# Kernel optimization log

Measured on AMD Instinct MI355X. Metric: run time of the kernel, lower is better.

The kernel has to match this reference:

```python
import jax, jax.numpy as jnp
import numpy as np

B, D, K, NUM_CLASSES = 8192, 512, 20, 1024
EPS = 1e-12  # torch F.normalize clamp


def setup_inputs() -> dict:
    key = jax.random.key(0)
    k1, k2 = jax.random.split(key)
    batch = jax.random.normal(k1, (B, D), dtype=jnp.float32)
    labels = jax.random.randint(k2, (B,), 0, NUM_CLASSES, dtype=jnp.int64 if jax.config.jax_enable_x64 else jnp.int32)
    return {"batch": batch, "labels": labels, "k": K}


def reference(batch, labels, k):
    # L2-normalize rows (F.normalize, p=2)
    norm = jnp.maximum(jnp.linalg.norm(batch, axis=1, keepdims=True), EPS)
    x = batch / norm
    cos = x @ x.T                                   # [B, B] cosine similarity
    min_value = cos.min() - 1.0                     # scalar, computed before diag fill
    bs = cos.shape[0]
    diag = jnp.eye(bs, dtype=bool)
    cos = jnp.where(diag, min_value, cos)           # fill_diagonal_(min_value)
    # argsort(-cos)[:, :k]  ==  top-k by similarity (self excluded via diag fill)
    top_vals, top_idx = jax.lax.top_k(cos, k)       # [B, k]
    # preds = (cos + 1)/2 gathered at neighbor indices == (top_vals + 1)/2
    preds = (top_vals + 1.0) * 0.5
    true_labels = (labels[top_idx] == labels[:, None]).astype(jnp.float32)  # [B, k]
    # nn.BCELoss with mean reduction; torch clamps each log term at -100
    logp = jnp.maximum(jnp.log(preds), -100.0)
    log1mp = jnp.maximum(jnp.log1p(-preds), -100.0)
    loss = -(true_labels * logp + (1.0 - true_labels) * log1mp)
    return loss.mean()
```

## Files before the change

kernel.cpp:

```cpp
#include <hip/hip_runtime.h>
#include <hip/hip_bf16.h>

#define NROWS 8192
#define DIM   512
#define KSEL  20
#define NSURV 384
#define NTRI  2080

typedef unsigned int u32;
typedef unsigned long long u64;
typedef short bf16x8 __attribute__((ext_vector_type(8)));
typedef float f32x4 __attribute__((ext_vector_type(4)));
typedef ushort u16x2 __attribute__((ext_vector_type(2)));

typedef const void __attribute__((address_space(1))) as1_void;
typedef void __attribute__((address_space(3))) as3_void;

__device__ __forceinline__ void async_ld16(const ushort* g, ushort* l) {
    __builtin_amdgcn_global_load_lds((as1_void*)g, (as3_void*)l, 16, 0, 0);
}

__device__ __forceinline__ ushort f2bf(float f) {
    u32 u = __float_as_uint(f);
    return (ushort)((u + 0x7FFFu + ((u >> 16) & 1u)) >> 16);
}

__device__ __forceinline__ u32 mono16(u32 r) {
    return r ^ (0x8000u | ((r >> 15) * 0x7FFFu));
}
__device__ __forceinline__ u32 mono2(u32 w) {
    return w ^ (0x80008000u | (((w >> 15) & 0x10001u) * 0x7FFFu));
}
__device__ __forceinline__ u32 mkey(float f) { return mono16((u32)f2bf(f)); }

__device__ __forceinline__ u32 pkmax(u32 a, u32 b) {
    union { u32 u; u16x2 v; } x, y; x.u = a; y.u = b;
    x.v = __builtin_elementwise_max(x.v, y.v);
    return x.u;
}
__device__ __forceinline__ u32 pkmin(u32 a, u32 b) {
    union { u32 u; u16x2 v; } x, y; x.u = a; y.u = b;
    x.v = __builtin_elementwise_min(x.v, y.v);
    return x.u;
}

__device__ __forceinline__ void tri_idx(int t, int& by, int& bx) {
    by = (int)((sqrtf(8.0f * (float)t + 1.0f) - 1.0f) * 0.5f);
    while ((by + 1) * (by + 2) / 2 <= t) ++by;
    while (by * (by + 1) / 2 > t) --by;
    bx = t - by * (by + 1) / 2;
}

__global__ __launch_bounds__(256) void k_norm(const float* __restrict__ x,
                                              ushort* __restrict__ xn) {
    int lane = threadIdx.x & 63;
    int wv   = threadIdx.x >> 6;
    int row  = blockIdx.x * 4 + wv;
    const float4* xr = (const float4*)(x + (size_t)row * DIM);
    float4 a = xr[2 * lane];
    float4 b = xr[2 * lane + 1];
    float ss = a.x*a.x + a.y*a.y + a.z*a.z + a.w*a.w
             + b.x*b.x + b.y*b.y + b.z*b.z + b.w*b.w;
    #pragma unroll
    for (int off = 32; off; off >>= 1) ss += __shfl_xor(ss, off);
    float sc = 1.0f / fmaxf(sqrtf(ss), 1e-12f);
    float v[8] = {a.x*sc, a.y*sc, a.z*sc, a.w*sc, b.x*sc, b.y*sc, b.z*sc, b.w*sc};
    union { ushort u[8]; uint4 q; } o;
    #pragma unroll
    for (int i = 0; i < 8; ++i) o.u[i] = f2bf(v[i]);
    *(uint4*)(xn + (size_t)row * DIM + lane * 8) = o.q;
}

__global__ __launch_bounds__(256) void k_gemm(const ushort* __restrict__ xn,
                                              ushort* __restrict__ C,
                                              ushort* __restrict__ M) {
    __shared__ ushort sh[128 * 128];
    ushort* lA = sh;
    ushort* lB = sh + 128 * 64;
    int tid  = threadIdx.x;
    int lane = tid & 63, wv = tid >> 6;
    int wr = wv >> 1, wc = wv & 1;
    int q = lane >> 4, m = lane & 15;
    int bx, by;
    tri_idx(blockIdx.x, by, bx);
    int grow0 = by * 128;
    int gcol0 = bx * 128;
    f32x4 acc[4][4] = {};

    int lr = lane >> 3;
    int lc = lane & 7;
    for (int kc = 0; kc < 8; ++kc) {
        #pragma unroll
        for (int t = 0; t < 4; ++t) {
            int rb  = wv * 32 + t * 8;
            int r   = rb + lr;
            int fch = lc ^ (r & 7);
            async_ld16(xn + (size_t)(grow0 + r) * DIM + kc * 64 + fch * 8, &lA[rb * 64]);
            async_ld16(xn + (size_t)(gcol0 + r) * DIM + kc * 64 + fch * 8, &lB[rb * 64]);
        }
        __syncthreads();
        #pragma unroll
        for (int s = 0; s < 2; ++s) {
            bf16x8 af[4], bfr[4];
            #pragma unroll
            for (int i = 0; i < 4; ++i) {
                int ra = wr * 64 + i * 16 + m;
                af[i]  = *(const bf16x8*)&lA[ra * 64 + (((s * 4 + q) ^ (ra & 7)) * 8)];
                int rb2 = wc * 64 + i * 16 + m;
                bfr[i] = *(const bf16x8*)&lB[rb2 * 64 + (((s * 4 + q) ^ (rb2 & 7)) * 8)];
            }
            #pragma unroll
            for (int i = 0; i < 4; ++i)
                #pragma unroll
                for (int j = 0; j < 4; ++j)
                    acc[i][j] = __builtin_amdgcn_mfma_f32_16x16x32_bf16(af[i], bfr[j], acc[i][j], 0, 0, 0);
        }
        __syncthreads();
    }

    float cmf[4] = {-3.0f, -3.0f, -3.0f, -3.0f};
    #pragma unroll
    for (int i = 0; i < 4; ++i) {
        float rmf[4] = {-3.0f, -3.0f, -3.0f, -3.0f};
        int rloc = wr * 64 + i * 16 + q * 4;
        #pragma unroll
        for (int j = 0; j < 4; ++j) {
            int cl = wc * 64 + j * 16 + m;
            int c  = gcol0 + cl;
            #pragma unroll
            for (int reg = 0; reg < 4; ++reg) {
                int r    = rloc + reg;
                int grw  = grow0 + r;
                float a  = acc[i][j][reg];
                bool dg  = (grw == c);
                float mv = dg ? -3.0f : a;
                rmf[reg] = fmaxf(rmf[reg], mv);
                cmf[j]   = fmaxf(cmf[j], mv);
                int D = r * 64 + ((cl >> 1) ^ (q << 3));
                sh[D * 2 + (cl & 1)] = dg ? (ushort)0xC040 : f2bf(a);
            }
        }
        u32 p01 = mkey(rmf[0]) | (mkey(rmf[1]) << 16);
        u32 p23 = mkey(rmf[2]) | (mkey(rmf[3]) << 16);
        #pragma unroll
        for (int off = 1; off <= 8; off <<= 1) {
            p01 = pkmax(p01, (u32)__shfl_xor((int)p01, off));
            p23 = pkmax(p23, (u32)__shfl_xor((int)p23, off));
        }
        if (m == 0) {
            size_t mb = (size_t)(grow0 + rloc) * 128 + bx * 2 + wc;
            M[mb]       = (ushort)(p01 & 0xFFFFu);
            M[mb + 128] = (ushort)(p01 >> 16);
            M[mb + 256] = (ushort)(p23 & 0xFFFFu);
            M[mb + 384] = (ushort)(p23 >> 16);
        }
    }
    if (bx != by) {
        u32 q01 = mkey(cmf[0]) | (mkey(cmf[1]) << 16);
        u32 q23 = mkey(cmf[2]) | (mkey(cmf[3]) << 16);
        q01 = pkmax(q01, (u32)__shfl_xor((int)q01, 16));
        q01 = pkmax(q01, (u32)__shfl_xor((int)q01, 32));
        q23 = pkmax(q23, (u32)__shfl_xor((int)q23, 16));
        q23 = pkmax(q23, (u32)__shfl_xor((int)q23, 32));
        if (q == 0) {
            int gc = gcol0 + wc * 64 + m;
            int sg = by * 2 + wr;
            M[(size_t)(gc +  0) * 128 + sg] = (ushort)(q01 & 0xFFFFu);
            M[(size_t)(gc + 16) * 128 + sg] = (ushort)(q01 >> 16);
            M[(size_t)(gc + 32) * 128 + sg] = (ushort)(q23 & 0xFFFFu);
            M[(size_t)(gc + 48) * 128 + sg] = (ushort)(q23 >> 16);
        }
    }
    __syncthreads();

    int tr = tid >> 4;
    int tc = tid & 15;
    #pragma unroll
    for (int p = 0; p < 8; ++p) {
        int r  = p * 16 + tr;
        int qr = (r >> 2) & 3;
        uint4 v = *(const uint4*)&sh[(r * 64 + ((tc * 4) ^ (qr << 3))) * 2];
        *(uint4*)&C[(size_t)(by * 128 + r) * NROWS + gcol0 + tc * 8] = v;
    }
}

__global__ __launch_bounds__(256) void k_thresh(const ushort* __restrict__ M,
                                                ushort* __restrict__ T) {
    int lane = threadIdx.x & 63;
    int wv   = threadIdx.x >> 6;
    int row  = blockIdx.x * 4 + wv;
    u32 pm  = *(const u32*)&M[(size_t)row * 128 + 2 * lane];
    u32 klo = pm & 0xFFFFu, khi = pm >> 16;
    u32 Tv = 0;
    #pragma unroll
    for (int b = 15; b >= 0; --b) {
        u32 cand = Tv | (1u << b);
        int c = __popcll(__ballot(klo >= cand)) + __popcll(__ballot(khi >= cand));
        if (c >= KSEL) Tv = cand;
    }
    if (Tv == 0) Tv = 1;
    if (lane == 0) T[row] = (ushort)Tv;
}

__global__ __launch_bounds__(256) void k_scan(const ushort* __restrict__ C,
                                              const ushort* __restrict__ T,
                                              u32* __restrict__ lists,
                                              u32* __restrict__ cnts) {
    int by, bx;
    tri_idx(blockIdx.x, by, bx);
    int tid = threadIdx.x;
    int tr  = tid >> 4;
    int gc  = bx * 128 + (tid & 15) * 8;
    bool diag = (bx == by);
    uint4 tq = *(const uint4*)&T[gc];
    u32 ts[4] = { tq.x, tq.y, tq.z, tq.w };
    u32 pmn = pkmin(pkmin(ts[0], ts[1]), pkmin(ts[2], ts[3]));
    u32 tmn = min(pmn & 0xFFFFu, pmn >> 16);
    #pragma unroll
    for (int p = 0; p < 8; ++p) {
        int gr = by * 128 + p * 16 + tr;
        uint4 v = *(const uint4*)&C[(size_t)gr * NROWS + gc];
        u32 k0 = mono2(v.x), k1 = mono2(v.y), k2 = mono2(v.z), k3 = mono2(v.w);
        u32 pmx = pkmax(pkmax(k0, k1), pkmax(k2, k3));
        u32 mx  = max(pmx & 0xFFFFu, pmx >> 16);
        u32 Tr  = (u32)T[gr];
        u32 ks[4] = { k0, k1, k2, k3 };
        if (mx >= Tr) {
            #pragma unroll
            for (int h = 0; h < 4; ++h) {
                u32 kA = ks[h] & 0xFFFFu, kB = ks[h] >> 16;
                if (kA >= Tr) { u32 o = atomicAdd(&cnts[gr], 1u); if (o < NSURV) lists[(size_t)gr * NSURV + o] = (kA << 16) | (u32)(gc + 2 * h); }
                if (kB >= Tr) { u32 o = atomicAdd(&cnts[gr], 1u); if (o < NSURV) lists[(size_t)gr * NSURV + o] = (kB << 16) | (u32)(gc + 2 * h + 1); }
            }
        }
        if (!diag && mx >= tmn) {
            #pragma unroll
            for (int h = 0; h < 4; ++h) {
                u32 kA = ks[h] & 0xFFFFu, kB = ks[h] >> 16;
                u32 tA = ts[h] & 0xFFFFu, tB = ts[h] >> 16;
                int cA = gc + 2 * h, cB = cA + 1;
                if (kA >= tA) { u32 o = atomicAdd(&cnts[cA], 1u); if (o < NSURV) lists[(size_t)cA * NSURV + o] = (kA << 16) | (u32)gr; }
                if (kB >= tB) { u32 o = atomicAdd(&cnts[cB], 1u); if (o < NSURV) lists[(size_t)cB * NSURV + o] = (kB << 16) | (u32)gr; }
            }
        }
    }
}

__global__ __launch_bounds__(256) void k_topk(const u32* __restrict__ lists,
                                              const u32* __restrict__ cnts,
                                              const int* __restrict__ labels,
                                              float* __restrict__ partials) {
    int lane = threadIdx.x & 63;
    int wv   = threadIdx.x >> 6;
    int row  = blockIdx.x * 4 + wv;
    u32 cnt = min(cnts[row], (u32)NSURV);
    const u32* L = lists + (size_t)row * NSURV;
    int mylab = labels[row];
    float loss = 0.0f;

    if (cnt <= 64u) {
        u32 gg  = ((u32)lane < cnt) ? L[lane] : 0u;
        u32 key = gg >> 16;
        u32 V = 0;
        #pragma unroll
        for (int b = 15; b >= 0; --b) {
            u32 cand = V | (1u << b);
            if (__popcll(__ballot(key >= cand)) >= KSEL) V = cand;
        }
        int cgt  = __popcll(__ballot(key > V));
        int ceq  = __popcll(__ballot(gg != 0 && key == V));
        int need = KSEL - cgt;
        bool incl;
        if (ceq == need) {
            incl = (gg != 0) && (key >= V);
        } else {
            u32 col = gg & 0xFFFFu;
            bool tie = (gg != 0) && (key == V);
            u32 Cv = 0;
            #pragma unroll
            for (int b = 15; b >= 0; --b) {
                u32 cand2 = Cv | (1u << b);
                if (__popcll(__ballot(tie && col >= cand2)) >= need) Cv = cand2;
            }
            incl = (key > V) || (tie && col >= Cv);
        }
        if (incl) {
            u32 col = gg & 0xFFFFu;
            u32 raw = (key & 0x8000u) ? (key ^ 0x8000u) : (key ^ 0xFFFFu);
            float v = __uint_as_float(raw << 16);
            float p = (v + 1.0f) * 0.5f;
            bool tm = (labels[col] == mylab);
            loss -= tm ? fmaxf(logf(p), -100.0f) : fmaxf(log1pf(-p), -100.0f);
        }
    } else {
        u32 g[6];
        #pragma unroll
        for (int j = 0; j < 6; ++j) {
            u32 idx = (u32)lane + (u32)j * 64u;
            g[j] = (idx < cnt) ? L[idx] : 0u;
        }
        u32 V = 0;
        #pragma unroll
        for (int b = 15; b >= 0; --b) {
            u32 cand = V | (1u << b);
            int c = 0;
            #pragma unroll
            for (int j = 0; j < 6; ++j)
                c += __popcll(__ballot((g[j] >> 16) >= cand));
            if (c >= KSEL) V = cand;
        }
        int cgt = 0, ceq = 0;
        #pragma unroll
        for (int j = 0; j < 6; ++j) {
            cgt += __popcll(__ballot(g[j] != 0 && (g[j] >> 16) > V));
            ceq += __popcll(__ballot(g[j] != 0 && (g[j] >> 16) == V));
        }
        int need = KSEL - cgt;
        bool all_ties = (ceq == need);
        #pragma unroll
        for (int j = 0; j < 6; ++j) {
            u32 key = g[j] >> 16, col = g[j] & 0xFFFFu;
            if (g[j] != 0 && (key > V || (all_ties && key == V))) {
                u32 raw = (key & 0x8000u) ? (key ^ 0x8000u) : (key ^ 0xFFFFu);
                float v = __uint_as_float(raw << 16);
                float p = (v + 1.0f) * 0.5f;
                bool tm = (labels[col] == mylab);
                loss -= tm ? fmaxf(logf(p), -100.0f) : fmaxf(log1pf(-p), -100.0f);
            }
        }
        if (!all_ties) {
            for (int r = 0; r < need; ++r) {
                u32 best = 0;
                #pragma unroll
                for (int j = 0; j < 6; ++j) {
                    u32 c2 = (g[j] != 0 && (g[j] >> 16) == V) ? ((g[j] & 0xFFFFu) + 1u) : 0u;
                    best = max(best, c2);
                }
                #pragma unroll
                for (int off = 32; off; off >>= 1) best = max(best, (u32)__shfl_xor((int)best, off));
                #pragma unroll
                for (int j = 0; j < 6; ++j) {
                    if (g[j] != 0 && (g[j] >> 16) == V && ((g[j] & 0xFFFFu) + 1u) == best) {
                        u32 col = g[j] & 0xFFFFu;
                        u32 raw = (V & 0x8000u) ? (V ^ 0x8000u) : (V ^ 0xFFFFu);
                        float v = __uint_as_float(raw << 16);
                        float p = (v + 1.0f) * 0.5f;
                        bool tm = (labels[col] == mylab);
                        loss -= tm ? fmaxf(logf(p), -100.0f) : fmaxf(log1pf(-p), -100.0f);
                        g[j] = 0;
                    }
                }
            }
        }
    }

    #pragma unroll
    for (int off = 32; off; off >>= 1) loss += __shfl_xor(loss, off);
    if (lane == 0) partials[row] = loss;
}

__global__ __launch_bounds__(256) void k_final(const float* __restrict__ partials,
                                               float* __restrict__ out) {
    __shared__ float s[4];
    int tid = threadIdx.x, lane = tid & 63, wvi = tid >> 6;
    const float4* p4 = (const float4*)partials;
    float sum = 0.0f;
    #pragma unroll
    for (int i = 0; i < 8; ++i) {
        float4 v = p4[tid + i * 256];
        sum += v.x + v.y + v.z + v.w;
    }
    #pragma unroll
    for (int off = 32; off; off >>= 1) sum += __shfl_xor(sum, off);
    if (lane == 0) s[wvi] = sum;
    __syncthreads();
    if (tid == 0) out[0] = (s[0] + s[1] + s[2] + s[3]) * (1.0f / (float)(NROWS * KSEL));
}

extern "C" void kernel_launch(void* const* d_in, const int* in_sizes, int n_in,
                              void* d_out, int out_size, void* d_ws, size_t ws_size,
                              hipStream_t stream) {
    const float* batch  = (const float*)d_in[0];
    const int*   labels = (const int*)d_in[1];

    ushort* xn = (ushort*)d_ws;
    ushort* C  = xn + (size_t)NROWS * DIM;

    char* scr = (char*)d_in[0];
    ushort* M        = (ushort*)scr;
    ushort* T        = (ushort*)(scr + (2u << 20));
    u32*    cnts     = (u32*)  (scr + (2u << 20) + (64u << 10));
    float*  partials = (float*)(scr + (2u << 20) + (128u << 10));
    u32*    lists    = (u32*)  (scr + (4u << 20));

    k_norm<<<NROWS / 4, 256, 0, stream>>>(batch, xn);
    hipMemsetAsync(cnts, 0, NROWS * sizeof(u32), stream);
    k_gemm  <<<NTRI,      256, 0, stream>>>(xn, C, M);
    k_thresh<<<NROWS / 4, 256, 0, stream>>>(M, T);
    k_scan  <<<NTRI,      256, 0, stream>>>(C, T, lists, cnts);
    k_topk  <<<NROWS / 4, 256, 0, stream>>>(lists, cnts, labels, partials);
    k_final <<<1,         256, 0, stream>>>(partials, (float*)d_out);
}
```

Measured before the change: 185.2 us.

## Store GEMM tiles in MFMA fragment order and scan them in that layout

The GEMM epilogue now writes each 128x128 bf16 tile straight to a per-block packed buffer in MFMA accumulator order. This removes the LDS staging pass, its extra barrier and the transposing row-major store. The scan kernel reads the packed tile contiguously and rebuilds row and column indices from the fragment layout. It fetches per-element row and column thresholds instead of per-row thresholds plus a column minimum. Stores become 8-byte per lane rather than 16-byte coalesced rows, and the scan's index math and threshold loads grow.

```diff
diff --git a/kernel.cpp b/kernel.cpp
--- a/kernel.cpp
+++ b/kernel.cpp
@@ -49,6 +49,11 @@
     while ((by + 1) * (by + 2) / 2 <= t) ++by;
     while (by * (by + 1) / 2 > t) --by;
     bx = t - by * (by + 1) / 2;
+}
+
+__device__ __forceinline__ void append(u32* lists, u32* cnts, int row, u32 val) {
+    u32 o = atomicAdd(&cnts[row], 1u);
+    if (o < NSURV) lists[(size_t)row * NSURV + o] = val;
 }
 
 __global__ __launch_bounds__(256) void k_norm(const float* __restrict__ x,
@@ -74,7 +79,7 @@
 __global__ __launch_bounds__(256) void k_gemm(const ushort* __restrict__ xn,
                                               ushort* __restrict__ C,
                                               ushort* __restrict__ M) {
-    __shared__ ushort sh[128 * 128];
+    __shared__ ushort sh[2 * 128 * 64];
     ushort* lA = sh;
     ushort* lB = sh + 128 * 64;
     int tid  = threadIdx.x;
@@ -118,6 +123,7 @@
         __syncthreads();
     }
 
+    size_t tb = (size_t)blockIdx.x * 16384;
     float cmf[4] = {-3.0f, -3.0f, -3.0f, -3.0f};
     #pragma unroll
     for (int i = 0; i < 4; ++i) {
@@ -127,18 +133,20 @@
         for (int j = 0; j < 4; ++j) {
             int cl = wc * 64 + j * 16 + m;
             int c  = gcol0 + cl;
+            ushort sv[4];
             #pragma unroll
             for (int reg = 0; reg < 4; ++reg) {
-                int r    = rloc + reg;
-                int grw  = grow0 + r;
+                int grw  = grow0 + rloc + reg;
                 float a  = acc[i][j][reg];
                 bool dg  = (grw == c);
                 float mv = dg ? -3.0f : a;
                 rmf[reg] = fmaxf(rmf[reg], mv);
                 cmf[j]   = fmaxf(cmf[j], mv);
-                int D = r * 64 + ((cl >> 1) ^ (q << 3));
-                sh[D * 2 + (cl & 1)] = dg ? (ushort)0xC040 : f2bf(a);
-            }
+                sv[reg]  = dg ? (ushort)0xC040 : f2bf(a);
+            }
+            uint2 o = { (u32)sv[0] | ((u32)sv[1] << 16),
+                        (u32)sv[2] | ((u32)sv[3] << 16) };
+            *(uint2*)&C[tb + (size_t)(((wv * 16 + i * 4 + j) * 64) + lane) * 4] = o;
         }
         u32 p01 = mkey(rmf[0]) | (mkey(rmf[1]) << 16);
         u32 p23 = mkey(rmf[2]) | (mkey(rmf[3]) << 16);
@@ -171,17 +179,6 @@
             M[(size_t)(gc + 48) * 128 + sg] = (ushort)(q23 >> 16);
         }
     }
-    __syncthreads();
-
-    int tr = tid >> 4;
-    int tc = tid & 15;
-    #pragma unroll
-    for (int p = 0; p < 8; ++p) {
-        int r  = p * 16 + tr;
-        int qr = (r >> 2) & 3;
-        uint4 v = *(const uint4*)&sh[(r * 64 + ((tc * 4) ^ (qr << 3))) * 2];
-        *(uint4*)&C[(size_t)(by * 128 + r) * NROWS + gcol0 + tc * 8] = v;
-    }
 }
 
 __global__ __launch_bounds__(256) void k_thresh(const ushort* __restrict__ M,
@@ -208,39 +205,45 @@
                                               u32* __restrict__ cnts) {
     int by, bx;
     tri_idx(blockIdx.x, by, bx);
+    const ushort* tile = C + (size_t)blockIdx.x * 16384;
     int tid = threadIdx.x;
-    int tr  = tid >> 4;
-    int gc  = bx * 128 + (tid & 15) * 8;
     bool diag = (bx == by);
-    uint4 tq = *(const uint4*)&T[gc];
-    u32 ts[4] = { tq.x, tq.y, tq.z, tq.w };
-    u32 pmn = pkmin(pkmin(ts[0], ts[1]), pkmin(ts[2], ts[3]));
-    u32 tmn = min(pmn & 0xFFFFu, pmn >> 16);
-    #pragma unroll
-    for (int p = 0; p < 8; ++p) {
-        int gr = by * 128 + p * 16 + tr;
-        uint4 v = *(const uint4*)&C[(size_t)gr * NROWS + gc];
+    #pragma unroll
+    for (int s = 0; s < 8; ++s) {
+        int e0 = s * 2048 + tid * 8;
+        uint4 v = *(const uint4*)&tile[e0];
+        int sub   = e0 >> 8;
+        int wv2   = sub >> 4, ii = (sub >> 2) & 3, jj = sub & 3;
+        int lane0 = (e0 >> 2) & 63;
+        int qq = lane0 >> 4, m0 = lane0 & 15;
+        int gr0 = by * 128 + (wv2 >> 1) * 64 + ii * 16 + qq * 4;
+        int gc0 = bx * 128 + (wv2 & 1) * 64 + jj * 16 + m0;
+        uint2 trw = *(const uint2*)&T[gr0];
+        u32   tc2 = *(const u32*)&T[gc0];
         u32 k0 = mono2(v.x), k1 = mono2(v.y), k2 = mono2(v.z), k3 = mono2(v.w);
         u32 pmx = pkmax(pkmax(k0, k1), pkmax(k2, k3));
         u32 mx  = max(pmx & 0xFFFFu, pmx >> 16);
-        u32 Tr  = (u32)T[gr];
-        u32 ks[4] = { k0, k1, k2, k3 };
-        if (mx >= Tr) {
-            #pragma unroll
-            for (int h = 0; h < 4; ++h) {
-                u32 kA = ks[h] & 0xFFFFu, kB = ks[h] >> 16;
-                if (kA >= Tr) { u32 o = atomicAdd(&cnts[gr], 1u); if (o < NSURV) lists[(size_t)gr * NSURV + o] = (kA << 16) | (u32)(gc + 2 * h); }
-                if (kB >= Tr) { u32 o = atomicAdd(&cnts[gr], 1u); if (o < NSURV) lists[(size_t)gr * NSURV + o] = (kB << 16) | (u32)(gc + 2 * h + 1); }
-            }
-        }
-        if (!diag && mx >= tmn) {
-            #pragma unroll
-            for (int h = 0; h < 4; ++h) {
-                u32 kA = ks[h] & 0xFFFFu, kB = ks[h] >> 16;
-                u32 tA = ts[h] & 0xFFFFu, tB = ts[h] >> 16;
-                int cA = gc + 2 * h, cB = cA + 1;
-                if (kA >= tA) { u32 o = atomicAdd(&cnts[cA], 1u); if (o < NSURV) lists[(size_t)cA * NSURV + o] = (kA << 16) | (u32)gr; }
-                if (kB >= tB) { u32 o = atomicAdd(&cnts[cB], 1u); if (o < NSURV) lists[(size_t)cB * NSURV + o] = (kB << 16) | (u32)gr; }
+        u32 rm2 = pkmin(trw.x, trw.y);
+        u32 rmn = min(rm2 & 0xFFFFu, rm2 >> 16);
+        u32 cmn = min(tc2 & 0xFFFFu, tc2 >> 16);
+        u32 thr = diag ? rmn : min(rmn, cmn);
+        if (mx < thr) continue;
+        u32 ks[4]  = { k0, k1, k2, k3 };
+        u32 trs[4] = { trw.x, trw.y, trw.x, trw.y };
+        u32 tcs[4] = { tc2 & 0xFFFFu, tc2 & 0xFFFFu, tc2 >> 16, tc2 >> 16 };
+        int cls[4] = { gc0, gc0, gc0 + 1, gc0 + 1 };
+        int rws[4] = { gr0, gr0 + 2, gr0, gr0 + 2 };
+        #pragma unroll
+        for (int h = 0; h < 4; ++h) {
+            u32 kA = ks[h] & 0xFFFFu, kB = ks[h] >> 16;
+            u32 tA = trs[h] & 0xFFFFu, tB = trs[h] >> 16;
+            int rA = rws[h], rB = rws[h] + 1, cc = cls[h];
+            if (kA >= tA) append(lists, cnts, rA, (kA << 16) | (u32)cc);
+            if (kB >= tB) append(lists, cnts, rB, (kB << 16) | (u32)cc);
+            if (!diag) {
+                u32 tc = tcs[h];
+                if (kA >= tc) append(lists, cnts, cc, (kA << 16) | (u32)rA);
+                if (kB >= tc) append(lists, cnts, cc, (kB << 16) | (u32)rB);
             }
         }
     }
```

New measurement: 177.5 us. 4.2% less time.
